# Kernel optimization log

Measured on AMD Instinct MI355X. Metric: run time of the kernel, lower is better.

## Reference

```python
import jax, jax.numpy as jnp
import numpy as np

B, N, E, H = 8, 2048, 1024, 16
D = E // H

def setup_inputs() -> dict:
    key = jax.random.key(0)
    kx, kw1, kb1, kw2, kb2 = jax.random.split(key, 5)
    scale = 0.02
    return {
        "x": jax.random.normal(kx, (B, N, E), dtype=jnp.float32),
        "Wqkv": jax.random.normal(kw1, (3 * E, E), dtype=jnp.float32) * scale,
        "bqkv": jax.random.normal(kb1, (3 * E,), dtype=jnp.float32) * scale,
        "Wo": jax.random.normal(kw2, (E, E), dtype=jnp.float32) * scale,
        "bo": jax.random.normal(kb2, (E,), dtype=jnp.float32) * scale,
    }

def reference(x, Wqkv, bqkv, Wo, bo):
    b, n, e = x.shape
    h, d = H, D
    # qkv projection: torch Linear is x @ W.T + b
    qkv = x @ Wqkv.T + bqkv                                   # [B,N,3E]
    qkv = qkv.reshape(b, n, 3, h, d).transpose(2, 0, 3, 1, 4)  # [3,B,H,N,D]
    q, k, v = qkv[0], qkv[1], qkv[2]                           # each [B,H,N,D]
    # NOTE: replicates the original's einsum labeling exactly: with q,k of
    # shape [B,H,N,D], 'nqhd,nkhd->nhqk' contracts over D and yields [B,N,H,H]
    # (softmax over the head axis), matching the torch source bit-for-bit.
    energy = jnp.einsum('nqhd,nkhd->nhqk', q, k)               # [B,N,H,H]
    attention = jax.nn.softmax(energy / jnp.sqrt(jnp.float32(e)), axis=-1)
    out = jnp.einsum('nhql,nlhd->nqhd', attention, v)          # [B,H,N,D]
    out = out.reshape(b, n, e)                                 # same raw-buffer reshape as torch
    return out @ Wo.T + bo
```

## Files before the change

kernel.cpp:

```cpp
#include <hip/hip_runtime.h>
#include <hip/hip_bf16.h>
#include <stdint.h>


typedef __attribute__((ext_vector_type(8))) short short8;
typedef __attribute__((ext_vector_type(8))) unsigned short ushort8;
typedef __attribute__((ext_vector_type(4))) unsigned short ushort4v;
typedef __attribute__((ext_vector_type(4))) float floatx4;

__device__ __forceinline__ unsigned short f2bf(float f) {
  union { float f; uint32_t u; } x; x.f = f;
  uint32_t u = x.u;
  return (unsigned short)((u + 0x7fffu + ((u >> 16) & 1u)) >> 16);
}

__global__ __launch_bounds__(256) void cvt_all(const float* __restrict__ x,
                                               const float* __restrict__ w1,
                                               const float* __restrict__ w2,
                                               unsigned short* __restrict__ xb,
                                               unsigned short* __restrict__ w1b,
                                               unsigned short* __restrict__ w2b) {
  int i = blockIdx.x * 256 + threadIdx.x;
  const float* src;
  unsigned short* dst;
  if (i < 2097152) {
    src = x; dst = xb;
  } else if (i < 2097152 + 393216) {
    i -= 2097152; src = w1; dst = w1b;
  } else {
    i -= 2490368; src = w2; dst = w2b;
  }
  long base = (long)i * 8;
  const float4* p = (const float4*)(src + base);
  float4 a = p[0], b = p[1];
  ushort8 r;
  r[0] = f2bf(a.x); r[1] = f2bf(a.y); r[2] = f2bf(a.z); r[3] = f2bf(a.w);
  r[4] = f2bf(b.x); r[5] = f2bf(b.y); r[6] = f2bf(b.z); r[7] = f2bf(b.w);
  *(ushort8*)(dst + base) = r;
}

__device__ __forceinline__ void gl2lds16(const void* g, void* l) {
  __builtin_amdgcn_global_load_lds(
      (const uint32_t __attribute__((address_space(1)))*)g,
      (uint32_t __attribute__((address_space(3)))*)(uint32_t)(uintptr_t)l,
      16, 0, 0);
}

template <bool OUT_BF16>
__device__ __forceinline__ void gemm256_core(const unsigned short* __restrict__ A,
                                             const unsigned short* __restrict__ Bm,
                                             const float* __restrict__ bias,
                                             void* __restrict__ Cout,
                                             int K, int ncols, int ldc) {
  __shared__ __align__(16) char lds[131072];
  char* lA = lds;
  char* lB = lds + 65536;

  const int id = blockIdx.x;
  const int local = id % (8 * ncols);
  const int brow = (id / (8 * ncols)) * 8 + (local & 7);
  const int bcol = local >> 3;
  const long row0 = (long)brow * 256;
  const long col0 = (long)bcol * 256;

  const int tid = threadIdx.x;
  const int lane = tid & 63;
  const int wave = tid >> 6;
  const int wm = wave >> 2;
  const int wn = wave & 3;
  const int l15 = lane & 15;
  const int lk = lane >> 4;

  float bv[4];
#pragma unroll
  for (int n = 0; n < 4; ++n) bv[n] = bias[col0 + wn * 64 + n * 16 + l15];
  asm volatile("s_waitcnt vmcnt(0)" ::: "memory");

  const int trow = tid >> 2;
  const int gch = (tid & 3) ^ ((tid >> 3) & 3);
  const unsigned short* gA = A + (row0 + trow) * (long)K + gch * 8;
  const unsigned short* gB = Bm + (col0 + trow) * (long)K + gch * 8;
  const long rstep = (long)128 * K;
  char* dA = lA + tid * 16;
  char* dB = lB + tid * 16;

  const int ch = ((lk ^ ((l15 >> 1) & 3)) << 4);
  const int aoff = (wm * 128 + l15) * 64 + ch;
  const int boff = (wn * 64 + l15) * 64 + ch;

  floatx4 acc[8][4] = {};
  const int NT = K >> 5;

#pragma unroll
  for (int t = 0; t < 3; ++t) {
    const long ko = (long)t * 32;
    gl2lds16(gA + ko, dA + t * 16384);
    gl2lds16(gA + rstep + ko, dA + t * 16384 + 8192);
    gl2lds16(gB + ko, dB + t * 16384);
    gl2lds16(gB + rstep + ko, dB + t * 16384 + 8192);
  }
  asm volatile("s_waitcnt vmcnt(8)" ::: "memory");
  __builtin_amdgcn_s_barrier();

#pragma unroll 1
  for (int kt = 0; kt < NT; ++kt) {
    const char* bufA = lA + (kt & 3) * 16384;
    const char* bufB = lB + (kt & 3) * 16384;
    const bool stage = (kt + 3 < NT);
    const long ko = (long)(kt + 3) * 32;
    const int sb = ((kt + 3) & 3) * 16384;

    short8 af[8], bfr[4];
#pragma unroll
    for (int n = 0; n < 4; ++n) bfr[n] = *(const short8*)(bufB + boff + n * 1024);
    af[0] = *(const short8*)(bufA + aoff + 0 * 1024);
    af[1] = *(const short8*)(bufA + aoff + 1 * 1024);
    af[2] = *(const short8*)(bufA + aoff + 2 * 1024);
    af[3] = *(const short8*)(bufA + aoff + 3 * 1024);
    asm volatile("s_waitcnt lgkmcnt(2)" ::: "memory");
    __builtin_amdgcn_sched_barrier(0);
    __builtin_amdgcn_s_setprio(1);
#pragma unroll
    for (int n = 0; n < 4; ++n) {
      acc[0][n] = __builtin_amdgcn_mfma_f32_16x16x32_bf16(af[0], bfr[n], acc[0][n], 0, 0, 0);
      acc[1][n] = __builtin_amdgcn_mfma_f32_16x16x32_bf16(af[1], bfr[n], acc[1][n], 0, 0, 0);
    }
    __builtin_amdgcn_s_setprio(0);
    af[4] = *(const short8*)(bufA + aoff + 4 * 1024);
    af[5] = *(const short8*)(bufA + aoff + 5 * 1024);
    asm volatile("s_waitcnt lgkmcnt(2)" ::: "memory");
    __builtin_amdgcn_sched_barrier(0);
    __builtin_amdgcn_s_setprio(1);
#pragma unroll
    for (int n = 0; n < 4; ++n) {
      acc[2][n] = __builtin_amdgcn_mfma_f32_16x16x32_bf16(af[2], bfr[n], acc[2][n], 0, 0, 0);
      acc[3][n] = __builtin_amdgcn_mfma_f32_16x16x32_bf16(af[3], bfr[n], acc[3][n], 0, 0, 0);
    }
    __builtin_amdgcn_s_setprio(0);
    af[6] = *(const short8*)(bufA + aoff + 6 * 1024);
    af[7] = *(const short8*)(bufA + aoff + 7 * 1024);
    if (stage) {
      gl2lds16(gA + ko, dA + sb);
      gl2lds16(gA + rstep + ko, dA + sb + 8192);
      gl2lds16(gB + ko, dB + sb);
      gl2lds16(gB + rstep + ko, dB + sb + 8192);
    }
    asm volatile("s_waitcnt lgkmcnt(2)" ::: "memory");
    __builtin_amdgcn_sched_barrier(0);
    __builtin_amdgcn_s_setprio(1);
#pragma unroll
    for (int n = 0; n < 4; ++n) {
      acc[4][n] = __builtin_amdgcn_mfma_f32_16x16x32_bf16(af[4], bfr[n], acc[4][n], 0, 0, 0);
      acc[5][n] = __builtin_amdgcn_mfma_f32_16x16x32_bf16(af[5], bfr[n], acc[5][n], 0, 0, 0);
    }
    __builtin_amdgcn_s_setprio(0);
    asm volatile("s_waitcnt lgkmcnt(0)" ::: "memory");
    __builtin_amdgcn_sched_barrier(0);
    __builtin_amdgcn_s_setprio(1);
#pragma unroll
    for (int n = 0; n < 4; ++n) {
      acc[6][n] = __builtin_amdgcn_mfma_f32_16x16x32_bf16(af[6], bfr[n], acc[6][n], 0, 0, 0);
      acc[7][n] = __builtin_amdgcn_mfma_f32_16x16x32_bf16(af[7], bfr[n], acc[7][n], 0, 0, 0);
    }
    __builtin_amdgcn_s_setprio(0);
    __builtin_amdgcn_sched_barrier(0);
    if (kt < NT - 3) { asm volatile("s_waitcnt vmcnt(8)" ::: "memory"); }
    else if (kt == NT - 3) { asm volatile("s_waitcnt vmcnt(4)" ::: "memory"); }
    else if (kt == NT - 2) { asm volatile("s_waitcnt vmcnt(0)" ::: "memory"); }
    __builtin_amdgcn_s_barrier();
  }

  const long crow0 = row0 + wm * 128 + lk * 4;
  const long ccol0 = col0 + wn * 64 + l15;
#pragma unroll
  for (int m = 0; m < 8; ++m)
#pragma unroll
    for (int n = 0; n < 4; ++n)
#pragma unroll
      for (int r = 0; r < 4; ++r) {
        const long row = crow0 + m * 16 + r;
        const long col = ccol0 + n * 16;
        const float v = acc[m][n][r] + bv[n];
        if (OUT_BF16)
          ((unsigned short*)Cout)[row * ldc + col] = f2bf(v);
        else
          ((float*)Cout)[row * ldc + col] = v;
      }
}

__global__ __launch_bounds__(512, 2) void gemm_qkv(const unsigned short* __restrict__ A,
                                                   const unsigned short* __restrict__ Bm,
                                                   const float* __restrict__ bias,
                                                   unsigned short* __restrict__ Cout, int K) {
  gemm256_core<true>(A, Bm, bias, Cout, K, 12, 3072);
}
__global__ __launch_bounds__(512, 2) void gemm_out(const unsigned short* __restrict__ A,
                                                   const unsigned short* __restrict__ Bm,
                                                   const float* __restrict__ bias,
                                                   float* __restrict__ Cout, int K) {
  gemm256_core<false>(A, Bm, bias, Cout, K, 4, 1024);
}

__global__ __launch_bounds__(256) void attn_kernel(const unsigned short* __restrict__ qkv,
                                                   unsigned short* __restrict__ out2) {
  __shared__ __align__(16) char lds[4 * 6144];
  const int tid = threadIdx.x;
  const int wave = tid >> 6;
  const int lane = tid & 63;
  const int token = blockIdx.x * 4 + wave;
  const int l15 = lane & 15;
  const int lk = lane >> 4;
  const int b = token >> 11;
  const int s = token & 2047;

  const char* gbase = (const char*)qkv + (long)token * 6144;
  char* lbase = lds + wave * 6144;
#pragma unroll
  for (int p = 0; p < 6; p++) {
    const int o = p * 1024 + lane * 16;
    const int row = o >> 7;
    const int chs = ((o >> 4) & 7) ^ (row & 7);
    const int src = (o & ~127) | (chs << 4);
    gl2lds16(gbase + src, lbase + o);
  }
  __syncthreads();

  const int sw = l15 & 7;
  const char* qrow = lbase + l15 * 128;
  const char* krow = lbase + 2048 + l15 * 128;
  const short8 kf0 = *(const short8*)(krow + ((lk ^ sw) << 4));
  const short8 kf1 = *(const short8*)(krow + (((lk + 4) ^ sw) << 4));
  const short8 qf0 = *(const short8*)(qrow + ((lk ^ sw) << 4));
  const short8 qf1 = *(const short8*)(qrow + (((lk + 4) ^ sw) << 4));
  floatx4 e = {};
  e = __builtin_amdgcn_mfma_f32_16x16x32_bf16(kf0, qf0, e, 0, 0, 0);
  e = __builtin_amdgcn_mfma_f32_16x16x32_bf16(kf1, qf1, e, 0, 0, 0);

  float ev[4];
#pragma unroll
  for (int r = 0; r < 4; ++r) ev[r] = e[r] * 0.03125f;
  float mx = fmaxf(fmaxf(ev[0], ev[1]), fmaxf(ev[2], ev[3]));
  mx = fmaxf(mx, __shfl_xor(mx, 16));
  mx = fmaxf(mx, __shfl_xor(mx, 32));
  float sum = 0.f;
#pragma unroll
  for (int r = 0; r < 4; ++r) { ev[r] = __expf(ev[r] - mx); sum += ev[r]; }
  sum += __shfl_xor(sum, 16);
  sum += __shfl_xor(sum, 32);
  const float inv = 1.f / sum;

  const uint32_t pa = (uint32_t)f2bf(ev[0] * inv) | ((uint32_t)f2bf(ev[1] * inv) << 16);
  const uint32_t pb = (uint32_t)f2bf(ev[2] * inv) | ((uint32_t)f2bf(ev[3] * inv) << 16);
  const int src0 = (l15 + 32 * lk) & 63;
  uint32_t w0 = __shfl(pa, src0);
  uint32_t w1 = __shfl(pb, src0);
  uint32_t w2 = __shfl(pa, (src0 + 16) & 63);
  uint32_t w3 = __shfl(pb, (src0 + 16) & 63);
  if (lk >= 2) { w0 = 0; w1 = 0; w2 = 0; w3 = 0; }
  union { short8 s8; uint32_t u[4]; } attf;
  attf.u[0] = w0; attf.u[1] = w1; attf.u[2] = w2; attf.u[3] = w3;

  const long orow = (long)b * 2048 + l15 * 128 + (s >> 4);
  unsigned short* op = out2 + orow * 1024 + (long)(s & 15) * 64;
#pragma unroll
  for (int c = 0; c < 4; ++c) {
    union { short8 s8; unsigned short us[8]; } vf;
    if (lk < 2) {
      const int byte_in = (c * 16 + l15) * 2;
#pragma unroll
      for (int i = 0; i < 8; ++i) {
        const int j = lk * 8 + i;
        const int chv = ((byte_in >> 4) ^ (j & 7));
        vf.us[i] = *(const unsigned short*)(lbase + 4096 + j * 128 + (chv << 4) +
                                            (byte_in & 15));
      }
    } else {
#pragma unroll
      for (int i = 0; i < 8; ++i) vf.us[i] = 0;
    }
    floatx4 o = {};
    o = __builtin_amdgcn_mfma_f32_16x16x32_bf16(vf.s8, attf.s8, o, 0, 0, 0);
    ushort4v r4;
#pragma unroll
    for (int r = 0; r < 4; ++r) r4[r] = f2bf(o[r]);
    *(ushort4v*)(op + c * 16 + lk * 4) = r4;
  }
}

extern "C" void kernel_launch(void* const* d_in, const int* in_sizes, int n_in,
                              void* d_out, int out_size, void* d_ws, size_t ws_size,
                              hipStream_t stream) {
  const float* x    = (const float*)d_in[0];
  const float* Wqkv = (const float*)d_in[1];
  const float* bqkv = (const float*)d_in[2];
  const float* Wo   = (const float*)d_in[3];
  const float* bo   = (const float*)d_in[4];
  float* out = (float*)d_out;

  char* ws = (char*)d_ws;
  unsigned short* x_bf    = (unsigned short*)(ws);
  unsigned short* wqkv_bf = (unsigned short*)(ws + 33554432);
  unsigned short* wo_bf   = (unsigned short*)(ws + 39845888);
  unsigned short* qkv_bf  = (unsigned short*)(ws + 41943040);
  unsigned short* out2_bf = (unsigned short*)(ws + 142606336);

  cvt_all<<<10240, 256, 0, stream>>>(x, Wqkv, Wo, x_bf, wqkv_bf, wo_bf);

  gemm_qkv<<<64 * 12, 512, 0, stream>>>(x_bf, wqkv_bf, bqkv, qkv_bf, 1024);

  attn_kernel<<<4096, 256, 0, stream>>>(qkv_bf, out2_bf);

  gemm_out<<<64 * 4, 512, 0, stream>>>(out2_bf, wo_bf, bo, out, 1024);
}
```

Before: 302.3 us.

## Load GEMM B operand straight from global into registers, bypassing LDS

The B tile no longer goes through shared memory. Each wave now loads its B fragments directly from global memory into registers, prefetching one k-step ahead, while A keeps its 4-deep LDS ring. This halves LDS use to 64KB, which could allow more resident blocks, and removes the B LDS reads. In exchange, each lane makes strided 16-byte global loads with only a single step of prefetch. Waves that share B columns also load it twice, and the loop now waits on those global loads every iteration.

Measured after the change: 371.2 us. 1.23x slower.

```diff
diff --git a/kernel.cpp b/kernel.cpp
--- a/kernel.cpp
+++ b/kernel.cpp
@@ -52,9 +52,7 @@
                                              const float* __restrict__ bias,
                                              void* __restrict__ Cout,
                                              int K, int ncols, int ldc) {
-  __shared__ __align__(16) char lds[131072];
-  char* lA = lds;
-  char* lB = lds + 65536;
+  __shared__ __align__(16) char lA[65536];
 
   const int id = blockIdx.x;
   const int local = id % (8 * ncols);
@@ -79,51 +77,50 @@
   const int trow = tid >> 2;
   const int gch = (tid & 3) ^ ((tid >> 3) & 3);
   const unsigned short* gA = A + (row0 + trow) * (long)K + gch * 8;
-  const unsigned short* gB = Bm + (col0 + trow) * (long)K + gch * 8;
   const long rstep = (long)128 * K;
   char* dA = lA + tid * 16;
-  char* dB = lB + tid * 16;
+
+  const unsigned short* gBf = Bm + (col0 + wn * 64 + l15) * (long)K + lk * 8;
 
   const int ch = ((lk ^ ((l15 >> 1) & 3)) << 4);
   const int aoff = (wm * 128 + l15) * 64 + ch;
-  const int boff = (wn * 64 + l15) * 64 + ch;
 
   floatx4 acc[8][4] = {};
   const int NT = K >> 5;
 
+  short8 bcur[4], bnxt[4];
 #pragma unroll
   for (int t = 0; t < 3; ++t) {
     const long ko = (long)t * 32;
     gl2lds16(gA + ko, dA + t * 16384);
     gl2lds16(gA + rstep + ko, dA + t * 16384 + 8192);
-    gl2lds16(gB + ko, dB + t * 16384);
-    gl2lds16(gB + rstep + ko, dB + t * 16384 + 8192);
-  }
-  asm volatile("s_waitcnt vmcnt(8)" ::: "memory");
+  }
+#pragma unroll
+  for (int n = 0; n < 4; ++n) bcur[n] = *(const short8*)(gBf + (long)n * 16 * K);
+  asm volatile("s_waitcnt vmcnt(0)" ::: "memory");
   __builtin_amdgcn_s_barrier();
 
 #pragma unroll 1
   for (int kt = 0; kt < NT; ++kt) {
     const char* bufA = lA + (kt & 3) * 16384;
-    const char* bufB = lB + (kt & 3) * 16384;
     const bool stage = (kt + 3 < NT);
+    const bool loadB = (kt + 1 < NT);
     const long ko = (long)(kt + 3) * 32;
     const int sb = ((kt + 3) & 3) * 16384;
 
-    short8 af[8], bfr[4];
-#pragma unroll
-    for (int n = 0; n < 4; ++n) bfr[n] = *(const short8*)(bufB + boff + n * 1024);
+    short8 af[8];
     af[0] = *(const short8*)(bufA + aoff + 0 * 1024);
     af[1] = *(const short8*)(bufA + aoff + 1 * 1024);
     af[2] = *(const short8*)(bufA + aoff + 2 * 1024);
     af[3] = *(const short8*)(bufA + aoff + 3 * 1024);
+    __builtin_amdgcn_sched_barrier(0);
     asm volatile("s_waitcnt lgkmcnt(2)" ::: "memory");
     __builtin_amdgcn_sched_barrier(0);
     __builtin_amdgcn_s_setprio(1);
 #pragma unroll
     for (int n = 0; n < 4; ++n) {
-      acc[0][n] = __builtin_amdgcn_mfma_f32_16x16x32_bf16(af[0], bfr[n], acc[0][n], 0, 0, 0);
-      acc[1][n] = __builtin_amdgcn_mfma_f32_16x16x32_bf16(af[1], bfr[n], acc[1][n], 0, 0, 0);
+      acc[0][n] = __builtin_amdgcn_mfma_f32_16x16x32_bf16(af[0], bcur[n], acc[0][n], 0, 0, 0);
+      acc[1][n] = __builtin_amdgcn_mfma_f32_16x16x32_bf16(af[1], bcur[n], acc[1][n], 0, 0, 0);
     }
     __builtin_amdgcn_s_setprio(0);
     af[4] = *(const short8*)(bufA + aoff + 4 * 1024);
@@ -133,25 +130,29 @@
     __builtin_amdgcn_s_setprio(1);
 #pragma unroll
     for (int n = 0; n < 4; ++n) {
-      acc[2][n] = __builtin_amdgcn_mfma_f32_16x16x32_bf16(af[2], bfr[n], acc[2][n], 0, 0, 0);
-      acc[3][n] = __builtin_amdgcn_mfma_f32_16x16x32_bf16(af[3], bfr[n], acc[3][n], 0, 0, 0);
+      acc[2][n] = __builtin_amdgcn_mfma_f32_16x16x32_bf16(af[2], bcur[n], acc[2][n], 0, 0, 0);
+      acc[3][n] = __builtin_amdgcn_mfma_f32_16x16x32_bf16(af[3], bcur[n], acc[3][n], 0, 0, 0);
     }
     __builtin_amdgcn_s_setprio(0);
     af[6] = *(const short8*)(bufA + aoff + 6 * 1024);
     af[7] = *(const short8*)(bufA + aoff + 7 * 1024);
+    if (loadB) {
+#pragma unroll
+      for (int n = 0; n < 4; ++n)
+        bnxt[n] = *(const short8*)(gBf + (long)n * 16 * K + (kt + 1) * 32);
+    }
     if (stage) {
       gl2lds16(gA + ko, dA + sb);
       gl2lds16(gA + rstep + ko, dA + sb + 8192);
-      gl2lds16(gB + ko, dB + sb);
-      gl2lds16(gB + rstep + ko, dB + sb + 8192);
-    }
+    }
+    __builtin_amdgcn_sched_barrier(0);
     asm volatile("s_waitcnt lgkmcnt(2)" ::: "memory");
     __builtin_amdgcn_sched_barrier(0);
     __builtin_amdgcn_s_setprio(1);
 #pragma unroll
     for (int n = 0; n < 4; ++n) {
-      acc[4][n] = __builtin_amdgcn_mfma_f32_16x16x32_bf16(af[4], bfr[n], acc[4][n], 0, 0, 0);
-      acc[5][n] = __builtin_amdgcn_mfma_f32_16x16x32_bf16(af[5], bfr[n], acc[5][n], 0, 0, 0);
+      acc[4][n] = __builtin_amdgcn_mfma_f32_16x16x32_bf16(af[4], bcur[n], acc[4][n], 0, 0, 0);
+      acc[5][n] = __builtin_amdgcn_mfma_f32_16x16x32_bf16(af[5], bcur[n], acc[5][n], 0, 0, 0);
     }
     __builtin_amdgcn_s_setprio(0);
     asm volatile("s_waitcnt lgkmcnt(0)" ::: "memory");
@@ -159,14 +160,17 @@
     __builtin_amdgcn_s_setprio(1);
 #pragma unroll
     for (int n = 0; n < 4; ++n) {
-      acc[6][n] = __builtin_amdgcn_mfma_f32_16x16x32_bf16(af[6], bfr[n], acc[6][n], 0, 0, 0);
-      acc[7][n] = __builtin_amdgcn_mfma_f32_16x16x32_bf16(af[7], bfr[n], acc[7][n], 0, 0, 0);
+      acc[6][n] = __builtin_amdgcn_mfma_f32_16x16x32_bf16(af[6], bcur[n], acc[6][n], 0, 0, 0);
+      acc[7][n] = __builtin_amdgcn_mfma_f32_16x16x32_bf16(af[7], bcur[n], acc[7][n], 0, 0, 0);
     }
     __builtin_amdgcn_s_setprio(0);
     __builtin_amdgcn_sched_barrier(0);
-    if (kt < NT - 3) { asm volatile("s_waitcnt vmcnt(8)" ::: "memory"); }
-    else if (kt == NT - 3) { asm volatile("s_waitcnt vmcnt(4)" ::: "memory"); }
-    else if (kt == NT - 2) { asm volatile("s_waitcnt vmcnt(0)" ::: "memory"); }
+    if (kt < NT - 3) { asm volatile("s_waitcnt vmcnt(2)" ::: "memory"); }
+    else if (kt < NT - 1) { asm volatile("s_waitcnt vmcnt(0)" ::: "memory"); }
+    if (loadB) {
+#pragma unroll
+      for (int n = 0; n < 4; ++n) bcur[n] = bnxt[n];
+    }
     __builtin_amdgcn_s_barrier();
   }
 
```

## Restructure GEMM main loop into 8-phase ping-pong schedule with 64-wide K tiles

Applied to the files above, without the earlier changes.

Rewrites the 256x256 GEMM core's pipeline. It now uses two 64-KB LDS buffers holding 64-wide K tiles split into halves, replacing the 4-slot ring of 32-wide tiles. Each iteration runs eight phases of 16 MFMAs, each bracketed by barriers, interleaving one global-to-LDS stage per phase with fragment reads. The aim is a finer schedule of LDS loads, global prefetch and MFMA issue across waves, in the style of a ping-pong scheme. It adds many more workgroup barriers and changes the accumulator row mapping, which the epilogue reorders to match.

Result: no change. 298.0 us (-1.4%).

```diff
diff --git a/kernel.cpp b/kernel.cpp
--- a/kernel.cpp
+++ b/kernel.cpp
@@ -53,8 +53,6 @@
                                              void* __restrict__ Cout,
                                              int K, int ncols, int ldc) {
   __shared__ __align__(16) char lds[131072];
-  char* lA = lds;
-  char* lB = lds + 65536;
 
   const int id = blockIdx.x;
   const int local = id % (8 * ncols);
@@ -70,6 +68,7 @@
   const int wn = wave & 3;
   const int l15 = lane & 15;
   const int lk = lane >> 4;
+  const int tid16 = tid * 16;
 
   float bv[4];
 #pragma unroll
@@ -81,111 +80,125 @@
   const unsigned short* gA = A + (row0 + trow) * (long)K + gch * 8;
   const unsigned short* gB = Bm + (col0 + trow) * (long)K + gch * 8;
   const long rstep = (long)128 * K;
-  char* dA = lA + tid * 16;
-  char* dB = lB + tid * 16;
-
-  const int ch = ((lk ^ ((l15 >> 1) & 3)) << 4);
-  const int aoff = (wm * 128 + l15) * 64 + ch;
-  const int boff = (wn * 64 + l15) * 64 + ch;
+
+#define STAGE_A(kt, h) do { \
+    const unsigned short* s_ = gA + (kt) * 64 + (h) * 32; \
+    char* d_ = lds + (((kt) & 1) << 16) + ((h) << 14) + tid16; \
+    gl2lds16(s_, d_); gl2lds16(s_ + rstep, d_ + 8192); } while (0)
+#define STAGE_B(kt, h) do { \
+    const unsigned short* s_ = gB + (kt) * 64 + (h) * 32; \
+    char* d_ = lds + (((kt) & 1) << 16) + 32768 + ((h) << 14) + tid16; \
+    gl2lds16(s_, d_); gl2lds16(s_ + 8192  - 8192 + rstep, d_ + 8192); } while (0)
+
+  const int chA = (lk ^ ((l15 >> 1) & 3)) << 4;
+  const int aBase = wm * 8192 + l15 * 64 + chA;
+  const int bBase = 32768 + wn * 4096 + l15 * 64 + chA;
+
+#define RD8(off) (*(const short8*)(lds + (off)))
+#define SBAR __builtin_amdgcn_sched_barrier(0)
+#define SYNC1 do { SBAR; __builtin_amdgcn_s_barrier(); \
+    asm volatile("s_waitcnt lgkmcnt(0)" ::: "memory"); SBAR; } while (0)
+#define MFMA16(M0) do { __builtin_amdgcn_s_setprio(1); \
+    _Pragma("unroll") for (int m = 0; m < 4; ++m) \
+    _Pragma("unroll") for (int n = 0; n < 4; ++n) \
+      acc[(M0) + m][n] = __builtin_amdgcn_mfma_f32_16x16x32_bf16(af[m], bf[n], acc[(M0) + m][n], 0, 0, 0); \
+    __builtin_amdgcn_s_setprio(0); SBAR; } while (0)
+#define VMC(N) asm volatile("s_waitcnt vmcnt(" #N ")" ::: "memory")
+#define EBAR __builtin_amdgcn_s_barrier()
 
   floatx4 acc[8][4] = {};
-  const int NT = K >> 5;
-
-#pragma unroll
-  for (int t = 0; t < 3; ++t) {
-    const long ko = (long)t * 32;
-    gl2lds16(gA + ko, dA + t * 16384);
-    gl2lds16(gA + rstep + ko, dA + t * 16384 + 8192);
-    gl2lds16(gB + ko, dB + t * 16384);
-    gl2lds16(gB + rstep + ko, dB + t * 16384 + 8192);
+  const int NT = K >> 6;
+  const int NI = NT >> 1;
+
+  STAGE_A(0, 0); STAGE_B(0, 0);
+  STAGE_A(0, 1); STAGE_B(0, 1);
+  STAGE_A(1, 0); STAGE_B(1, 0);
+  VMC(8);
+  EBAR;
+
+#pragma unroll 1
+  for (int I = 0; I < NI; ++I) {
+    const int t = 2 * I;
+    const bool more = (I + 1 < NI);
+    short8 af[4], bf[4];
+
+#pragma unroll
+    for (int n = 0; n < 4; ++n) bf[n] = RD8(bBase + n * 1024);
+#pragma unroll
+    for (int m = 0; m < 4; ++m) af[m] = RD8(aBase + m * 1024);
+    STAGE_A(t + 1, 1);
+    SYNC1; MFMA16(0); EBAR;
+
+#pragma unroll
+    for (int m = 0; m < 4; ++m) af[m] = RD8(aBase + 4096 + m * 1024);
+    STAGE_B(t + 1, 1);
+    SYNC1; MFMA16(4); VMC(8); EBAR;
+
+#pragma unroll
+    for (int n = 0; n < 4; ++n) bf[n] = RD8(16384 + bBase + n * 1024);
+#pragma unroll
+    for (int m = 0; m < 4; ++m) af[m] = RD8(16384 + aBase + m * 1024);
+    if (more) STAGE_A(t + 2, 0);
+    SYNC1; MFMA16(0); EBAR;
+
+#pragma unroll
+    for (int m = 0; m < 4; ++m) af[m] = RD8(16384 + aBase + 4096 + m * 1024);
+    if (more) STAGE_B(t + 2, 0);
+    SYNC1; MFMA16(4);
+    if (more) { VMC(8); } else { VMC(4); }
+    EBAR;
+
+#pragma unroll
+    for (int n = 0; n < 4; ++n) bf[n] = RD8(65536 + bBase + n * 1024);
+#pragma unroll
+    for (int m = 0; m < 4; ++m) af[m] = RD8(65536 + aBase + m * 1024);
+    if (more) STAGE_A(t + 2, 1);
+    SYNC1; MFMA16(0); EBAR;
+
+#pragma unroll
+    for (int m = 0; m < 4; ++m) af[m] = RD8(65536 + aBase + 4096 + m * 1024);
+    if (more) STAGE_B(t + 2, 1);
+    SYNC1; MFMA16(4);
+    if (more) { VMC(8); } else { VMC(0); }
+    EBAR;
+
+#pragma unroll
+    for (int n = 0; n < 4; ++n) bf[n] = RD8(65536 + 16384 + bBase + n * 1024);
+#pragma unroll
+    for (int m = 0; m < 4; ++m) af[m] = RD8(65536 + 16384 + aBase + m * 1024);
+    if (more) STAGE_A(t + 3, 0);
+    SYNC1; MFMA16(0); EBAR;
+
+#pragma unroll
+    for (int m = 0; m < 4; ++m) af[m] = RD8(65536 + 16384 + aBase + 4096 + m * 1024);
+    if (more) STAGE_B(t + 3, 0);
+    SYNC1; MFMA16(4);
+    if (more) { VMC(8); }
+    EBAR;
   }
-  asm volatile("s_waitcnt vmcnt(8)" ::: "memory");
-  __builtin_amdgcn_s_barrier();
-
-#pragma unroll 1
-  for (int kt = 0; kt < NT; ++kt) {
-    const char* bufA = lA + (kt & 3) * 16384;
-    const char* bufB = lB + (kt & 3) * 16384;
-    const bool stage = (kt + 3 < NT);
-    const long ko = (long)(kt + 3) * 32;
-    const int sb = ((kt + 3) & 3) * 16384;
-
-    short8 af[8], bfr[4];
-#pragma unroll
-    for (int n = 0; n < 4; ++n) bfr[n] = *(const short8*)(bufB + boff + n * 1024);
-    af[0] = *(const short8*)(bufA + aoff + 0 * 1024);
-    af[1] = *(const short8*)(bufA + aoff + 1 * 1024);
-    af[2] = *(const short8*)(bufA + aoff + 2 * 1024);
-    af[3] = *(const short8*)(bufA + aoff + 3 * 1024);
-    asm volatile("s_waitcnt lgkmcnt(2)" ::: "memory");
-    __builtin_amdgcn_sched_barrier(0);
-    __builtin_amdgcn_s_setprio(1);
-#pragma unroll
-    for (int n = 0; n < 4; ++n) {
-      acc[0][n] = __builtin_amdgcn_mfma_f32_16x16x32_bf16(af[0], bfr[n], acc[0][n], 0, 0, 0);
-      acc[1][n] = __builtin_amdgcn_mfma_f32_16x16x32_bf16(af[1], bfr[n], acc[1][n], 0, 0, 0);
-    }
-    __builtin_amdgcn_s_setprio(0);
-    af[4] = *(const short8*)(bufA + aoff + 4 * 1024);
-    af[5] = *(const short8*)(bufA + aoff + 5 * 1024);
-    asm volatile("s_waitcnt lgkmcnt(2)" ::: "memory");
-    __builtin_amdgcn_sched_barrier(0);
-    __builtin_amdgcn_s_setprio(1);
-#pragma unroll
-    for (int n = 0; n < 4; ++n) {
-      acc[2][n] = __builtin_amdgcn_mfma_f32_16x16x32_bf16(af[2], bfr[n], acc[2][n], 0, 0, 0);
-      acc[3][n] = __builtin_amdgcn_mfma_f32_16x16x32_bf16(af[3], bfr[n], acc[3][n], 0, 0, 0);
-    }
-    __builtin_amdgcn_s_setprio(0);
-    af[6] = *(const short8*)(bufA + aoff + 6 * 1024);
-    af[7] = *(const short8*)(bufA + aoff + 7 * 1024);
-    if (stage) {
-      gl2lds16(gA + ko, dA + sb);
-      gl2lds16(gA + rstep + ko, dA + sb + 8192);
-      gl2lds16(gB + ko, dB + sb);
-      gl2lds16(gB + rstep + ko, dB + sb + 8192);
-    }
-    asm volatile("s_waitcnt lgkmcnt(2)" ::: "memory");
-    __builtin_amdgcn_sched_barrier(0);
-    __builtin_amdgcn_s_setprio(1);
-#pragma unroll
-    for (int n = 0; n < 4; ++n) {
-      acc[4][n] = __builtin_amdgcn_mfma_f32_16x16x32_bf16(af[4], bfr[n], acc[4][n], 0, 0, 0);
-      acc[5][n] = __builtin_amdgcn_mfma_f32_16x16x32_bf16(af[5], bfr[n], acc[5][n], 0, 0, 0);
-    }
-    __builtin_amdgcn_s_setprio(0);
-    asm volatile("s_waitcnt lgkmcnt(0)" ::: "memory");
-    __builtin_amdgcn_sched_barrier(0);
-    __builtin_amdgcn_s_setprio(1);
-#pragma unroll
-    for (int n = 0; n < 4; ++n) {
-      acc[6][n] = __builtin_amdgcn_mfma_f32_16x16x32_bf16(af[6], bfr[n], acc[6][n], 0, 0, 0);
-      acc[7][n] = __builtin_amdgcn_mfma_f32_16x16x32_bf16(af[7], bfr[n], acc[7][n], 0, 0, 0);
-    }
-    __builtin_amdgcn_s_setprio(0);
-    __builtin_amdgcn_sched_barrier(0);
-    if (kt < NT - 3) { asm volatile("s_waitcnt vmcnt(8)" ::: "memory"); }
-    else if (kt == NT - 3) { asm volatile("s_waitcnt vmcnt(4)" ::: "memory"); }
-    else if (kt == NT - 2) { asm volatile("s_waitcnt vmcnt(0)" ::: "memory"); }
-    __builtin_amdgcn_s_barrier();
-  }
-
-  const long crow0 = row0 + wm * 128 + lk * 4;
-  const long ccol0 = col0 + wn * 64 + l15;
-#pragma unroll
-  for (int m = 0; m < 8; ++m)
+
+#pragma unroll
+  for (int midx = 0; midx < 8; ++midx)
 #pragma unroll
     for (int n = 0; n < 4; ++n)
 #pragma unroll
       for (int r = 0; r < 4; ++r) {
-        const long row = crow0 + m * 16 + r;
-        const long col = ccol0 + n * 16;
-        const float v = acc[m][n][r] + bv[n];
+        const long row = row0 + wm * 128 + (midx >> 2) * 64 + (midx & 3) * 16 + lk * 4 + r;
+        const long col = col0 + wn * 64 + n * 16 + l15;
+        const float v = acc[midx][n][r] + bv[n];
         if (OUT_BF16)
           ((unsigned short*)Cout)[row * ldc + col] = f2bf(v);
         else
           ((float*)Cout)[row * ldc + col] = v;
       }
+#undef STAGE_A
+#undef STAGE_B
+#undef RD8
+#undef SBAR
+#undef SYNC1
+#undef MFMA16
+#undef VMC
+#undef EBAR
 }
 
 __global__ __launch_bounds__(512, 2) void gemm_qkv(const unsigned short* __restrict__ A,
```

## Write attention output token-contiguous and fold permutation into out-projection A loads

Applied to the files above, without the earlier changes.

The attention kernel now writes each token's 16x64 output block contiguously instead of scattering it into the raw-buffer-reshaped layout. The out-projection GEMM absorbs that permutation through a permuted A-operand addressing scheme, with adjusted row step and k offsets. This makes the attention stores coalesced. In exchange, the GEMM's A-tile global loads become strided across tokens, which may hurt load efficiency.

New measurement: 291.0 us. 1.04x faster.

```diff
diff --git a/kernel.cpp b/kernel.cpp
--- a/kernel.cpp
+++ b/kernel.cpp
@@ -46,7 +46,7 @@
       16, 0, 0);
 }
 
-template <bool OUT_BF16>
+template <bool OUT_BF16, bool PERM_A>
 __device__ __forceinline__ void gemm256_core(const unsigned short* __restrict__ A,
                                              const unsigned short* __restrict__ Bm,
                                              const float* __restrict__ bias,
@@ -78,7 +78,17 @@
 
   const int trow = tid >> 2;
   const int gch = (tid & 3) ^ ((tid >> 3) & 3);
-  const unsigned short* gA = A + (row0 + trow) * (long)K + gch * 8;
+  const unsigned short* gA;
+  long rstepA;
+  if (PERM_A) {
+    const int b_ = brow >> 3;
+    const int q_ = (brow * 2) & 15;
+    gA = A + ((long)((b_ << 11) | (trow << 4)) << 10) + q_ * 64 + gch * 8;
+    rstepA = 64;
+  } else {
+    gA = A + (row0 + trow) * (long)K + gch * 8;
+    rstepA = (long)128 * K;
+  }
   const unsigned short* gB = Bm + (col0 + trow) * (long)K + gch * 8;
   const long rstep = (long)128 * K;
   char* dA = lA + tid * 16;
@@ -93,11 +103,12 @@
 
 #pragma unroll
   for (int t = 0; t < 3; ++t) {
-    const long ko = (long)t * 32;
-    gl2lds16(gA + ko, dA + t * 16384);
-    gl2lds16(gA + rstep + ko, dA + t * 16384 + 8192);
-    gl2lds16(gB + ko, dB + t * 16384);
-    gl2lds16(gB + rstep + ko, dB + t * 16384 + 8192);
+    const long koA = PERM_A ? (long)((t >> 1) * 1024 + (t & 1) * 32) : (long)t * 32;
+    const long koB = (long)t * 32;
+    gl2lds16(gA + koA, dA + t * 16384);
+    gl2lds16(gA + rstepA + koA, dA + t * 16384 + 8192);
+    gl2lds16(gB + koB, dB + t * 16384);
+    gl2lds16(gB + rstep + koB, dB + t * 16384 + 8192);
   }
   asm volatile("s_waitcnt vmcnt(8)" ::: "memory");
   __builtin_amdgcn_s_barrier();
@@ -107,8 +118,10 @@
     const char* bufA = lA + (kt & 3) * 16384;
     const char* bufB = lB + (kt & 3) * 16384;
     const bool stage = (kt + 3 < NT);
-    const long ko = (long)(kt + 3) * 32;
-    const int sb = ((kt + 3) & 3) * 16384;
+    const int ks = kt + 3;
+    const long koA = PERM_A ? (long)((ks >> 1) * 1024 + (ks & 1) * 32) : (long)ks * 32;
+    const long koB = (long)ks * 32;
+    const int sb = (ks & 3) * 16384;
 
     short8 af[8], bfr[4];
 #pragma unroll
@@ -140,10 +153,10 @@
     af[6] = *(const short8*)(bufA + aoff + 6 * 1024);
     af[7] = *(const short8*)(bufA + aoff + 7 * 1024);
     if (stage) {
-      gl2lds16(gA + ko, dA + sb);
-      gl2lds16(gA + rstep + ko, dA + sb + 8192);
-      gl2lds16(gB + ko, dB + sb);
-      gl2lds16(gB + rstep + ko, dB + sb + 8192);
+      gl2lds16(gA + koA, dA + sb);
+      gl2lds16(gA + rstepA + koA, dA + sb + 8192);
+      gl2lds16(gB + koB, dB + sb);
+      gl2lds16(gB + rstep + koB, dB + sb + 8192);
     }
     asm volatile("s_waitcnt lgkmcnt(2)" ::: "memory");
     __builtin_amdgcn_sched_barrier(0);
@@ -192,13 +205,13 @@
                                                    const unsigned short* __restrict__ Bm,
                                                    const float* __restrict__ bias,
                                                    unsigned short* __restrict__ Cout, int K) {
-  gemm256_core<true>(A, Bm, bias, Cout, K, 12, 3072);
+  gemm256_core<true, false>(A, Bm, bias, Cout, K, 12, 3072);
 }
 __global__ __launch_bounds__(512, 2) void gemm_out(const unsigned short* __restrict__ A,
                                                    const unsigned short* __restrict__ Bm,
                                                    const float* __restrict__ bias,
                                                    float* __restrict__ Cout, int K) {
-  gemm256_core<false>(A, Bm, bias, Cout, K, 4, 1024);
+  gemm256_core<false, true>(A, Bm, bias, Cout, K, 4, 1024);
 }
 
 __global__ __launch_bounds__(256) void attn_kernel(const unsigned short* __restrict__ qkv,
@@ -210,8 +223,6 @@
   const int token = blockIdx.x * 4 + wave;
   const int l15 = lane & 15;
   const int lk = lane >> 4;
-  const int b = token >> 11;
-  const int s = token & 2047;
 
   const char* gbase = (const char*)qkv + (long)token * 6144;
   char* lbase = lds + wave * 6144;
@@ -260,8 +271,7 @@
   union { short8 s8; uint32_t u[4]; } attf;
   attf.u[0] = w0; attf.u[1] = w1; attf.u[2] = w2; attf.u[3] = w3;
 
-  const long orow = (long)b * 2048 + l15 * 128 + (s >> 4);
-  unsigned short* op = out2 + orow * 1024 + (long)(s & 15) * 64;
+  unsigned short* op = out2 + (long)token * 1024 + l15 * 64;
 #pragma unroll
   for (int c = 0; c < 4; ++c) {
     union { short8 s8; unsigned short us[8]; } vf;
```
